# Kernel optimization log

Hardware: AMD Instinct MI355X
Metric: run time of the kernel (lower is better)

The kernel has to match this reference:

```python
import jax, jax.numpy as jnp
import numpy as np

IN_FEATURES = 4096
OUT_FEATURES = 4096
NUM_FRAGMENTS = 16
FRAGMENT_SIZE = IN_FEATURES // NUM_FRAGMENTS  # 256
COMPRESSED = 512
BATCH = 8192


def setup_inputs() -> dict:
    key = jax.random.key(0)
    k0, k1, k2, k3, k4 = jax.random.split(key, 5)
    x = jax.random.normal(k0, (BATCH, IN_FEATURES), dtype=jnp.float32)
    selector_weights = jax.random.normal(k1, (NUM_FRAGMENTS, FRAGMENT_SIZE), dtype=jnp.float32) / np.sqrt(FRAGMENT_SIZE)
    expert_weights = jax.random.normal(k2, (NUM_FRAGMENTS, FRAGMENT_SIZE, OUT_FEATURES), dtype=jnp.float32) / np.sqrt(FRAGMENT_SIZE)
    # torch nn.Linear stores weight as [out, in]; y = x @ W.T
    compressor_w = jax.random.normal(k3, (COMPRESSED, IN_FEATURES), dtype=jnp.float32) / np.sqrt(IN_FEATURES)
    compressed_net_w = jax.random.normal(k4, (OUT_FEATURES, COMPRESSED), dtype=jnp.float32) / np.sqrt(COMPRESSED)
    return {
        'x': x,
        'selector_weights': selector_weights,
        'expert_weights': expert_weights,
        'compressor_w': compressor_w,
        'compressed_net_w': compressed_net_w,
    }


def reference(x, selector_weights, expert_weights, compressor_w, compressed_net_w):
    B = x.shape[0]
    # [B, F, s]
    x_frag = x.reshape(B, NUM_FRAGMENTS, FRAGMENT_SIZE)

    # --- selector ---
    scores = jnp.einsum('bfi,fi->bf', x_frag, selector_weights)
    probs = jax.nn.softmax(scores, axis=1)
    selected = jnp.argmax(probs, axis=1)  # [B] int, top-1 fragment per token

    # --- expert computation (top-1 dispatch, expressed as one-hot grouped GEMM) ---
    one_hot = jax.nn.one_hot(selected, NUM_FRAGMENTS, dtype=x.dtype)  # [B, F]
    # selected fragment's vector [B, s] times its expert matrix [s, O]
    expert_out = jnp.einsum('bf,bfi,fio->bo', one_hot, x_frag, expert_weights)

    # --- compressed residual path: mask out selected fragment's features ---
    # fragment_mapping expands one_hot to feature granularity; mask = 1 on non-selected features
    mask = 1.0 - jnp.repeat(one_hot, FRAGMENT_SIZE, axis=1)  # [B, in_features]
    masked = x * mask
    compressed = masked @ compressor_w.T        # [B, compressed]
    compressed_out = compressed @ compressed_net_w.T  # [B, out]

    return expert_out + compressed_out
```

## Files before the change

### kernel.cpp

```cpp
#include <hip/hip_runtime.h>
#include <stdint.h>

typedef unsigned short u16;
typedef __attribute__((ext_vector_type(4))) float  fvec4;
typedef __attribute__((ext_vector_type(4))) float  f32x4;
typedef __attribute__((ext_vector_type(8))) short  s16x8;
typedef __attribute__((ext_vector_type(4))) u16    u16x4;

#define AS1 __attribute__((address_space(1)))
#define AS3 __attribute__((address_space(3)))
#define MEMFENCE() asm volatile("" ::: "memory")

#define B_TOK   8192
#define NFRAG   16
#define FSZ     256
#define INF     4096
#define OUTF    4096
#define COMP    512
#define KCAT    768
#define CSTRIDE 64

__device__ __forceinline__ u16 f2bf(float f){
  union { float fv; unsigned int u; } v; v.fv = f;
  unsigned int u = v.u;
  u += 0x7fffu + ((u >> 16) & 1u);
  return (u16)(u >> 16);
}

__device__ __forceinline__ void async16(const void* g, void* l){
  __builtin_amdgcn_global_load_lds((const AS1 unsigned int*)g, (AS3 unsigned int*)l, 16, 0, 0);
}

__global__ void cast_bf16(const float* __restrict__ in, u16* __restrict__ out, int nquads){
  for (int i = blockIdx.x * blockDim.x + threadIdx.x; i < nquads; i += gridDim.x * blockDim.x){
    fvec4 v = ((const fvec4*)in)[i];
    u16x4 o; o.x = f2bf(v.x); o.y = f2bf(v.y); o.z = f2bf(v.z); o.w = f2bf(v.w);
    ((u16x4*)out)[i] = o;
  }
}

__global__ void transpose_cast_w(const float* __restrict__ W, u16* __restrict__ Wt){
  __shared__ u16 ldsT[64][72];
  const int e  = blockIdx.z;
  const int kt = blockIdx.y;
  const int nt = blockIdx.x;
  const int t  = threadIdx.x;
  const float* Wb = W + (size_t)e * FSZ * OUTF;

  const int tr = t >> 4;
  const int tc = t & 15;
  #pragma unroll
  for (int it = 0; it < 4; ++it){
    int k = it * 16 + tr;
    fvec4 v = *(const fvec4*)(Wb + (size_t)(kt * 64 + k) * OUTF + nt * 64 + tc * 4);
    ldsT[tc*4 + 0][k] = f2bf(v.x);
    ldsT[tc*4 + 1][k] = f2bf(v.y);
    ldsT[tc*4 + 2][k] = f2bf(v.z);
    ldsT[tc*4 + 3][k] = f2bf(v.w);
  }
  __syncthreads();
  u16* Wtb = Wt + (size_t)e * OUTF * FSZ;
  const int nr = t >> 3;
  const int nc = t & 7;
  #pragma unroll
  for (int it = 0; it < 2; ++it){
    int n = it * 32 + nr;
    s16x8 val = *(const s16x8*)&ldsT[n][nc * 8];
    *(s16x8*)(Wtb + (size_t)(nt * 64 + n) * FSZ + kt * 64 + nc * 8) = val;
  }
}

__global__ void prep_kernel(const float* __restrict__ x, const float* __restrict__ sw,
                            u16* __restrict__ masked, u16* __restrict__ Acat,
                            int* __restrict__ counts, int* __restrict__ tok_list){
  const int b = blockIdx.x;
  const int t = threadIdx.x;
  const int w = t >> 6;
  const int l = t & 63;
  const float* xr = x + (size_t)b * INF;
  const fvec4* xq  = (const fvec4*)xr;
  const fvec4* swq = (const fvec4*)sw;

  fvec4 v[4];
  float p[4];
  #pragma unroll
  for (int j = 0; j < 4; ++j){
    v[j] = xq[j * 256 + t];
    fvec4 wv = swq[(j * 4 + w) * 64 + l];
    p[j] = v[j].x * wv.x + v[j].y * wv.y + v[j].z * wv.z + v[j].w * wv.w;
  }
  #pragma unroll
  for (int m = 1; m < 64; m <<= 1){
    #pragma unroll
    for (int j = 0; j < 4; ++j) p[j] += __shfl_xor(p[j], m, 64);
  }

  __shared__ float sc[NFRAG];
  if (l == 0){
    #pragma unroll
    for (int j = 0; j < 4; ++j) sc[j * 4 + w] = p[j];
  }
  __syncthreads();

  float best = sc[0]; int sel = 0;
  #pragma unroll
  for (int i = 1; i < NFRAG; ++i){ if (sc[i] > best){ best = sc[i]; sel = i; } }

  if (t == 0){
    int pos = atomicAdd(&counts[sel * CSTRIDE], 1);
    tok_list[sel * B_TOK + pos] = b;
  }

  u16x4* mq = (u16x4*)(masked + (size_t)b * INF);
  #pragma unroll
  for (int j = 0; j < 4; ++j){
    const bool insel = ((j * 4 + w) == sel);
    u16x4 o;
    o.x = insel ? (u16)0 : f2bf(v[j].x);
    o.y = insel ? (u16)0 : f2bf(v[j].y);
    o.z = insel ? (u16)0 : f2bf(v[j].z);
    o.w = insel ? (u16)0 : f2bf(v[j].w);
    mq[j * 256 + t] = o;
    if (insel){
      u16x4 s;
      s.x = f2bf(v[j].x); s.y = f2bf(v[j].y); s.z = f2bf(v[j].z); s.w = f2bf(v[j].w);
      ((u16x4*)(Acat + (size_t)b * KCAT + COMP))[l] = s;
    }
  }
}

template<int EPI>
__global__ __launch_bounds__(256, 2)
void gemm_bt(const u16* __restrict__ A, int lda,
             const u16* __restrict__ B, int ldb,
             void* __restrict__ Cout, int ldc,
             int ktlen){
  __shared__ u16 Ab[2][128 * 64];
  __shared__ u16 Bb[2][128 * 64];

  const int t    = threadIdx.x;
  const int wv   = t >> 6;
  const int lane = t & 63;
  const int cx   = blockIdx.x;
  const int ry   = blockIdx.y;
  const int kt0  = blockIdx.z * ktlen;
  const int wr = wv >> 1, wc = wv & 1;
  const int l15 = lane & 15, lq = lane >> 4;

  auto stage = [&](int buf, int kt){
    const int k0 = (kt0 + kt) << 6;
    #pragma unroll
    for (int it = 0; it < 4; ++it){
      int G = it * 256 + wv * 64 + lane;
      int row = G >> 3;
      int g = (G & 7) ^ (row & 7);
      async16(A + (size_t)(ry * 128 + row) * lda + k0 + g * 8, &Ab[buf][(it * 256 + wv * 64) * 8]);
    }
    #pragma unroll
    for (int it = 0; it < 4; ++it){
      int G = it * 256 + wv * 64 + lane;
      int row = G >> 3;
      int g = (G & 7) ^ (row & 7);
      async16(B + (size_t)(cx * 128 + row) * ldb + k0 + g * 8, &Bb[buf][(it * 256 + wv * 64) * 8]);
    }
  };

  f32x4 acc[4][4];
  #pragma unroll
  for (int i = 0; i < 4; ++i)
    #pragma unroll
    for (int j = 0; j < 4; ++j){
      f32x4 z = {0.f, 0.f, 0.f, 0.f};
      acc[i][j] = z;
    }

  stage(0, 0);
  for (int kt = 0; kt < ktlen; ++kt){
    const int cur = kt & 1;
    if (kt + 1 < ktlen){
      stage(cur ^ 1, kt + 1);
      __builtin_amdgcn_sched_barrier(0);
      asm volatile("s_waitcnt vmcnt(8)" ::: "memory");
    } else {
      __builtin_amdgcn_sched_barrier(0);
      asm volatile("s_waitcnt vmcnt(0)" ::: "memory");
    }
    MEMFENCE(); __builtin_amdgcn_s_barrier(); MEMFENCE();

    #pragma unroll
    for (int kk = 0; kk < 2; ++kk){
      s16x8 af[4], bfr[4];
      #pragma unroll
      for (int i = 0; i < 4; ++i){
        int row = wr * 64 + i * 16 + l15;
        int sg  = (kk * 4 + lq) ^ (row & 7);
        af[i] = *(const s16x8*)&Ab[cur][row * 64 + sg * 8];
      }
      #pragma unroll
      for (int j = 0; j < 4; ++j){
        int row = wc * 64 + j * 16 + l15;
        int sg  = (kk * 4 + lq) ^ (row & 7);
        bfr[j] = *(const s16x8*)&Bb[cur][row * 64 + sg * 8];
      }
      #pragma unroll
      for (int i = 0; i < 4; ++i)
        #pragma unroll
        for (int j = 0; j < 4; ++j)
          acc[i][j] = __builtin_amdgcn_mfma_f32_16x16x32_bf16(af[i], bfr[j], acc[i][j], 0, 0, 0);
    }

    MEMFENCE(); __builtin_amdgcn_s_barrier(); MEMFENCE();
  }

  #pragma unroll
  for (int i = 0; i < 4; ++i){
    #pragma unroll
    for (int j = 0; j < 4; ++j){
      int rloc = wr * 64 + i * 16 + lq * 4;
      int col  = cx * 128 + wc * 64 + j * 16 + l15;
      #pragma unroll
      for (int r = 0; r < 4; ++r){
        int rit = rloc + r;
        if (EPI == 0){
          ((u16*)Cout)[(size_t)(ry * 128 + rit) * ldc + col] = f2bf(acc[i][j][r]);
        } else {
          atomicAdd((float*)Cout + (size_t)(ry * 128 + rit) * ldc + col, acc[i][j][r]);
        }
      }
    }
  }
}

__global__ void reduce_cast(const float* __restrict__ P, u16* __restrict__ Acat){
  const int n = B_TOK * COMP / 4;
  for (int i = blockIdx.x * blockDim.x + threadIdx.x; i < n; i += gridDim.x * blockDim.x){
    int row = i >> 7;
    int c   = i & 127;
    fvec4 v = ((const fvec4*)P)[i];
    u16x4 o; o.x = f2bf(v.x); o.y = f2bf(v.y); o.z = f2bf(v.z); o.w = f2bf(v.w);
    ((u16x4*)(Acat + (size_t)row * KCAT))[c] = o;
  }
}

__global__ __launch_bounds__(256, 2)
void gemm_fused(const u16* __restrict__ Acat, const u16* __restrict__ Db,
                const u16* __restrict__ Wt, float* __restrict__ out,
                const int* __restrict__ counts, const int* __restrict__ tok_list){
  __shared__ u16 Ab[2][128 * 64];
  __shared__ u16 Bb[2][128 * 64];
  __shared__ int rowtok[128];

  const int t    = threadIdx.x;
  const int wv   = t >> 6;
  const int lane = t & 63;
  const int cx   = blockIdx.x;
  const int e    = blockIdx.z;
  const int Me   = counts[e * CSTRIDE];
  const u16* Wte = Wt + (size_t)e * OUTF * FSZ;
  const int KT   = KCAT >> 6;
  const int wr = wv >> 1, wc = wv & 1;
  const int l15 = lane & 15, lq = lane >> 4;

  for (int ry = blockIdx.y; ry * 128 < Me; ry += (int)gridDim.y){
    if (t < 128){
      int r  = ry * 128 + t;
      int rc = (r < Me) ? r : (Me - 1);
      rowtok[t] = tok_list[e * B_TOK + rc];
    }
    __syncthreads();

    auto stage = [&](int buf, int kt){
      #pragma unroll
      for (int it = 0; it < 4; ++it){
        int G = it * 256 + wv * 64 + lane;
        int row = G >> 3;
        int g = (G & 7) ^ (row & 7);
        async16(Acat + (size_t)rowtok[row] * KCAT + kt * 64 + g * 8, &Ab[buf][(it * 256 + wv * 64) * 8]);
      }
      #pragma unroll
      for (int it = 0; it < 4; ++it){
        int G = it * 256 + wv * 64 + lane;
        int row = G >> 3;
        int g = (G & 7) ^ (row & 7);
        const u16* src;
        if (kt < 8) src = Db  + (size_t)(cx * 128 + row) * COMP + kt * 64 + g * 8;
        else        src = Wte + (size_t)(cx * 128 + row) * FSZ  + (kt - 8) * 64 + g * 8;
        async16(src, &Bb[buf][(it * 256 + wv * 64) * 8]);
      }
    };

    f32x4 acc[4][4];
    #pragma unroll
    for (int i = 0; i < 4; ++i)
      #pragma unroll
      for (int j = 0; j < 4; ++j){
        f32x4 z = {0.f, 0.f, 0.f, 0.f};
        acc[i][j] = z;
      }

    stage(0, 0);
    for (int kt = 0; kt < KT; ++kt){
      const int cur = kt & 1;
      if (kt + 1 < KT){
        stage(cur ^ 1, kt + 1);
        __builtin_amdgcn_sched_barrier(0);
        asm volatile("s_waitcnt vmcnt(8)" ::: "memory");
      } else {
        __builtin_amdgcn_sched_barrier(0);
        asm volatile("s_waitcnt vmcnt(0)" ::: "memory");
      }
      MEMFENCE(); __builtin_amdgcn_s_barrier(); MEMFENCE();

      #pragma unroll
      for (int kk = 0; kk < 2; ++kk){
        s16x8 af[4], bfr[4];
        #pragma unroll
        for (int i = 0; i < 4; ++i){
          int row = wr * 64 + i * 16 + l15;
          int sg  = (kk * 4 + lq) ^ (row & 7);
          af[i] = *(const s16x8*)&Ab[cur][row * 64 + sg * 8];
        }
        #pragma unroll
        for (int j = 0; j < 4; ++j){
          int row = wc * 64 + j * 16 + l15;
          int sg  = (kk * 4 + lq) ^ (row & 7);
          bfr[j] = *(const s16x8*)&Bb[cur][row * 64 + sg * 8];
        }
        #pragma unroll
        for (int i = 0; i < 4; ++i)
          #pragma unroll
          for (int j = 0; j < 4; ++j)
            acc[i][j] = __builtin_amdgcn_mfma_f32_16x16x32_bf16(af[i], bfr[j], acc[i][j], 0, 0, 0);
      }

      MEMFENCE(); __builtin_amdgcn_s_barrier(); MEMFENCE();
    }

    #pragma unroll
    for (int i = 0; i < 4; ++i){
      #pragma unroll
      for (int j = 0; j < 4; ++j){
        int rloc = wr * 64 + i * 16 + lq * 4;
        int col  = cx * 128 + wc * 64 + j * 16 + l15;
        #pragma unroll
        for (int r = 0; r < 4; ++r){
          int rit = rloc + r;
          out[(size_t)rowtok[rit] * OUTF + col] = acc[i][j][r];
        }
      }
    }
    __syncthreads();
  }
}

extern "C" void kernel_launch(void* const* d_in, const int* in_sizes, int n_in,
                              void* d_out, int out_size, void* d_ws, size_t ws_size,
                              hipStream_t stream){
  const float* x  = (const float*)d_in[0];
  const float* sw = (const float*)d_in[1];
  const float* W  = (const float*)d_in[2];
  const float* C  = (const float*)d_in[3];
  const float* D  = (const float*)d_in[4];
  float* out = (float*)d_out;

  char* w = (char*)d_ws;
  size_t off = 0;
  auto alloc = [&](size_t bytes) -> void* {
    void* p = w + off;
    off += (bytes + 255) & ~(size_t)255;
    return p;
  };
  u16* masked = (u16*)alloc((size_t)B_TOK * INF * 2);
  u16* Acat   = (u16*)alloc((size_t)B_TOK * KCAT * 2);
  u16* Cb     = (u16*)alloc((size_t)COMP * INF * 2);
  u16* Db     = (u16*)alloc((size_t)OUTF * COMP * 2);
  u16* Wt     = (u16*)alloc((size_t)NFRAG * OUTF * FSZ * 2);
  int* counts = (int*)alloc(NFRAG * CSTRIDE * sizeof(int));
  int* toks   = (int*)alloc((size_t)NFRAG * B_TOK * sizeof(int));
  float* comp_f32 = (float*)alloc((size_t)B_TOK * COMP * sizeof(float));
  const bool split = (off <= ws_size);

  hipMemsetAsync(counts, 0, NFRAG * CSTRIDE * sizeof(int), stream);

  cast_bf16<<<2048, 256, 0, stream>>>(C, Cb, (COMP * INF) / 4);
  cast_bf16<<<2048, 256, 0, stream>>>(D, Db, (OUTF * COMP) / 4);
  transpose_cast_w<<<dim3(64, 4, 16), 256, 0, stream>>>(W, Wt);
  prep_kernel<<<B_TOK, 256, 0, stream>>>(x, sw, masked, Acat, counts, toks);

  if (split){
    hipMemsetAsync(comp_f32, 0, (size_t)B_TOK * COMP * sizeof(float), stream);
    gemm_bt<4><<<dim3(COMP / 128, B_TOK / 128, 2), 256, 0, stream>>>(
        masked, INF, Cb, INF, comp_f32, COMP, 32);
    reduce_cast<<<1024, 256, 0, stream>>>(comp_f32, Acat);
  } else {
    gemm_bt<0><<<dim3(COMP / 128, B_TOK / 128, 1), 256, 0, stream>>>(
        masked, INF, Cb, INF, Acat, KCAT, 64);
  }

  gemm_fused<<<dim3(OUTF / 128, 8, NFRAG), 256, 0, stream>>>(
      Acat, Db, Wt, out, counts, toks);
}
```

Baseline: 471.2 us.

## Replace split-K compressor GEMM with 128x64-tile direct-write kernel and merge casts

```diff
diff --git a/kernel.cpp b/kernel.cpp
--- a/kernel.cpp
+++ b/kernel.cpp
@@ -31,11 +31,16 @@
   __builtin_amdgcn_global_load_lds((const AS1 unsigned int*)g, (AS3 unsigned int*)l, 16, 0, 0);
 }
 
-__global__ void cast_bf16(const float* __restrict__ in, u16* __restrict__ out, int nquads){
-  for (int i = blockIdx.x * blockDim.x + threadIdx.x; i < nquads; i += gridDim.x * blockDim.x){
-    fvec4 v = ((const fvec4*)in)[i];
+__global__ void cast2_bf16(const float* __restrict__ C, const float* __restrict__ D,
+                           u16* __restrict__ Cb, u16* __restrict__ Db){
+  const int nq = COMP * INF / 4;
+  for (int i = blockIdx.x * blockDim.x + threadIdx.x; i < 2 * nq; i += gridDim.x * blockDim.x){
+    const float* src = (i < nq) ? C : D;
+    u16* dst        = (i < nq) ? Cb : Db;
+    int k = (i < nq) ? i : (i - nq);
+    fvec4 v = ((const fvec4*)src)[k];
     u16x4 o; o.x = f2bf(v.x); o.y = f2bf(v.y); o.z = f2bf(v.z); o.w = f2bf(v.w);
-    ((u16x4*)out)[i] = o;
+    ((u16x4*)dst)[k] = o;
   }
 }
 
@@ -129,45 +134,40 @@
   }
 }
 
-template<int EPI>
-__global__ __launch_bounds__(256, 2)
-void gemm_bt(const u16* __restrict__ A, int lda,
-             const u16* __restrict__ B, int ldb,
-             void* __restrict__ Cout, int ldc,
-             int ktlen){
+__global__ __launch_bounds__(256, 3)
+void gemm_comp(const u16* __restrict__ A, const u16* __restrict__ B, u16* __restrict__ Cout){
   __shared__ u16 Ab[2][128 * 64];
-  __shared__ u16 Bb[2][128 * 64];
+  __shared__ u16 Bb[2][64 * 64];
 
   const int t    = threadIdx.x;
   const int wv   = t >> 6;
   const int lane = t & 63;
   const int cx   = blockIdx.x;
   const int ry   = blockIdx.y;
-  const int kt0  = blockIdx.z * ktlen;
-  const int wr = wv >> 1, wc = wv & 1;
   const int l15 = lane & 15, lq = lane >> 4;
+  const int KT = INF >> 6;
 
   auto stage = [&](int buf, int kt){
-    const int k0 = (kt0 + kt) << 6;
+    const int k0 = kt << 6;
     #pragma unroll
     for (int it = 0; it < 4; ++it){
       int G = it * 256 + wv * 64 + lane;
       int row = G >> 3;
       int g = (G & 7) ^ (row & 7);
-      async16(A + (size_t)(ry * 128 + row) * lda + k0 + g * 8, &Ab[buf][(it * 256 + wv * 64) * 8]);
-    }
-    #pragma unroll
-    for (int it = 0; it < 4; ++it){
+      async16(A + (size_t)(ry * 128 + row) * INF + k0 + g * 8, &Ab[buf][(it * 256 + wv * 64) * 8]);
+    }
+    #pragma unroll
+    for (int it = 0; it < 2; ++it){
       int G = it * 256 + wv * 64 + lane;
       int row = G >> 3;
       int g = (G & 7) ^ (row & 7);
-      async16(B + (size_t)(cx * 128 + row) * ldb + k0 + g * 8, &Bb[buf][(it * 256 + wv * 64) * 8]);
+      async16(B + (size_t)(cx * 64 + row) * INF + k0 + g * 8, &Bb[buf][(it * 256 + wv * 64) * 8]);
     }
   };
 
-  f32x4 acc[4][4];
-  #pragma unroll
-  for (int i = 0; i < 4; ++i)
+  f32x4 acc[2][4];
+  #pragma unroll
+  for (int i = 0; i < 2; ++i)
     #pragma unroll
     for (int j = 0; j < 4; ++j){
       f32x4 z = {0.f, 0.f, 0.f, 0.f};
@@ -175,12 +175,12 @@
     }
 
   stage(0, 0);
-  for (int kt = 0; kt < ktlen; ++kt){
+  for (int kt = 0; kt < KT; ++kt){
     const int cur = kt & 1;
-    if (kt + 1 < ktlen){
+    if (kt + 1 < KT){
       stage(cur ^ 1, kt + 1);
       __builtin_amdgcn_sched_barrier(0);
-      asm volatile("s_waitcnt vmcnt(8)" ::: "memory");
+      asm volatile("s_waitcnt vmcnt(6)" ::: "memory");
     } else {
       __builtin_amdgcn_sched_barrier(0);
       asm volatile("s_waitcnt vmcnt(0)" ::: "memory");
@@ -189,21 +189,21 @@
 
     #pragma unroll
     for (int kk = 0; kk < 2; ++kk){
-      s16x8 af[4], bfr[4];
-      #pragma unroll
-      for (int i = 0; i < 4; ++i){
-        int row = wr * 64 + i * 16 + l15;
+      s16x8 af[2], bfr[4];
+      #pragma unroll
+      for (int i = 0; i < 2; ++i){
+        int row = wv * 32 + i * 16 + l15;
         int sg  = (kk * 4 + lq) ^ (row & 7);
         af[i] = *(const s16x8*)&Ab[cur][row * 64 + sg * 8];
       }
       #pragma unroll
       for (int j = 0; j < 4; ++j){
-        int row = wc * 64 + j * 16 + l15;
+        int row = j * 16 + l15;
         int sg  = (kk * 4 + lq) ^ (row & 7);
         bfr[j] = *(const s16x8*)&Bb[cur][row * 64 + sg * 8];
       }
       #pragma unroll
-      for (int i = 0; i < 4; ++i)
+      for (int i = 0; i < 2; ++i)
         #pragma unroll
         for (int j = 0; j < 4; ++j)
           acc[i][j] = __builtin_amdgcn_mfma_f32_16x16x32_bf16(af[i], bfr[j], acc[i][j], 0, 0, 0);
@@ -213,32 +213,16 @@
   }
 
   #pragma unroll
-  for (int i = 0; i < 4; ++i){
+  for (int i = 0; i < 2; ++i){
     #pragma unroll
     for (int j = 0; j < 4; ++j){
-      int rloc = wr * 64 + i * 16 + lq * 4;
-      int col  = cx * 128 + wc * 64 + j * 16 + l15;
+      int rloc = wv * 32 + i * 16 + lq * 4;
+      int col  = cx * 64 + j * 16 + l15;
       #pragma unroll
       for (int r = 0; r < 4; ++r){
-        int rit = rloc + r;
-        if (EPI == 0){
-          ((u16*)Cout)[(size_t)(ry * 128 + rit) * ldc + col] = f2bf(acc[i][j][r]);
-        } else {
-          atomicAdd((float*)Cout + (size_t)(ry * 128 + rit) * ldc + col, acc[i][j][r]);
-        }
-      }
-    }
-  }
-}
-
-__global__ void reduce_cast(const float* __restrict__ P, u16* __restrict__ Acat){
-  const int n = B_TOK * COMP / 4;
-  for (int i = blockIdx.x * blockDim.x + threadIdx.x; i < n; i += gridDim.x * blockDim.x){
-    int row = i >> 7;
-    int c   = i & 127;
-    fvec4 v = ((const fvec4*)P)[i];
-    u16x4 o; o.x = f2bf(v.x); o.y = f2bf(v.y); o.z = f2bf(v.z); o.w = f2bf(v.w);
-    ((u16x4*)(Acat + (size_t)row * KCAT))[c] = o;
+        Cout[(size_t)(ry * 128 + rloc + r) * KCAT + col] = f2bf(acc[i][j][r]);
+      }
+    }
   }
 }
 
@@ -377,26 +361,15 @@
   u16* Wt     = (u16*)alloc((size_t)NFRAG * OUTF * FSZ * 2);
   int* counts = (int*)alloc(NFRAG * CSTRIDE * sizeof(int));
   int* toks   = (int*)alloc((size_t)NFRAG * B_TOK * sizeof(int));
-  float* comp_f32 = (float*)alloc((size_t)B_TOK * COMP * sizeof(float));
-  const bool split = (off <= ws_size);
 
   hipMemsetAsync(counts, 0, NFRAG * CSTRIDE * sizeof(int), stream);
 
-  cast_bf16<<<2048, 256, 0, stream>>>(C, Cb, (COMP * INF) / 4);
-  cast_bf16<<<2048, 256, 0, stream>>>(D, Db, (OUTF * COMP) / 4);
+  cast2_bf16<<<2048, 256, 0, stream>>>(C, D, Cb, Db);
   transpose_cast_w<<<dim3(64, 4, 16), 256, 0, stream>>>(W, Wt);
   prep_kernel<<<B_TOK, 256, 0, stream>>>(x, sw, masked, Acat, counts, toks);
 
-  if (split){
-    hipMemsetAsync(comp_f32, 0, (size_t)B_TOK * COMP * sizeof(float), stream);
-    gemm_bt<4><<<dim3(COMP / 128, B_TOK / 128, 2), 256, 0, stream>>>(
-        masked, INF, Cb, INF, comp_f32, COMP, 32);
-    reduce_cast<<<1024, 256, 0, stream>>>(comp_f32, Acat);
-  } else {
-    gemm_bt<0><<<dim3(COMP / 128, B_TOK / 128, 1), 256, 0, stream>>>(
-        masked, INF, Cb, INF, Acat, KCAT, 64);
-  }
-
-  gemm_fused<<<dim3(OUTF / 128, 8, NFRAG), 256, 0, stream>>>(
+  gemm_comp<<<dim3(COMP / 64, B_TOK / 128), 256, 0, stream>>>(masked, Cb, Acat);
+
+  gemm_fused<<<dim3(OUTF / 128, 4, NFRAG), 256, 0, stream>>>(
       Acat, Db, Wt, out, counts, toks);
 }
```

New measurement: 466.2 us. Within noise of the previous version (-1.1%).
